# Performance work log

Hardware: AMD Instinct MI355X
Metric: run time of the kernel (lower is better)

The kernel has to match this reference:

```python
import jax, jax.numpy as jnp
import numpy as np

N_NODES = 100000


def _gcn_conv(x, w, b, edge_index, n):
    # Linear transform
    x = x @ w + b
    # Add self loops
    loops = jnp.tile(jnp.arange(n, dtype=edge_index.dtype), (2, 1))
    ei = jnp.concatenate([edge_index, loops], axis=1)
    src, tgt = ei[0], ei[1]
    # Degree of source nodes (every node has a self loop -> deg >= 1)
    deg = jax.ops.segment_sum(jnp.ones(src.shape, x.dtype), src, num_segments=n)
    dinv = deg ** -0.5
    norm = dinv[src] * dinv[tgt]  # [E+N]
    # Gather-scale-scatter: out[t] += norm_e * x[s]
    msgs = norm[:, None] * x[src]  # [E+N, out_ch]
    return jax.ops.segment_sum(msgs, tgt, num_segments=n)


def setup_inputs() -> dict:
    key = jax.random.key(0)
    ks = jax.random.split(key, 6)
    n, f_in, hid, n_cls, e = N_NODES, 512, 16, 40, 3200000
    x = jax.random.normal(ks[0], (n, f_in), dtype=jnp.float32)
    edge_index = jax.random.randint(ks[1], (2, e), 0, n, dtype=jnp.int64)
    w1 = jax.random.normal(ks[2], (f_in, hid), dtype=jnp.float32) * (1.0 / np.sqrt(f_in))
    b1 = jax.random.normal(ks[3], (hid,), dtype=jnp.float32) * 0.01
    w2 = jax.random.normal(ks[4], (hid, n_cls), dtype=jnp.float32) * (1.0 / np.sqrt(hid))
    b2 = jax.random.normal(ks[5], (n_cls,), dtype=jnp.float32) * 0.01
    return {"x": x, "edge_index": edge_index, "w1": w1, "b1": b1, "w2": w2, "b2": b2}


def reference(x, edge_index, w1, b1, w2, b2):
    n = x.shape[0]
    h = _gcn_conv(x, w1, b1, edge_index, n)
    h = jax.nn.relu(h)
    # dropout is identity in eval mode (F.dropout with training=False)
    h = _gcn_conv(h, w2, b2, edge_index, n)
    return jax.nn.log_softmax(h, axis=1)
```

## Files before the change

kernel.cpp:

```cpp
#include <hip/hip_runtime.h>
#include <hip/hip_fp16.h>
#include <cstdint>

#define FIN 512
#define HID 16
#define NCLS 40
#define SHIFT 8
#define NBCAP 512
#define NBLK 512
#define BR 64
#define KC 32
#define CAP 12288
#define FCAP 12288

typedef int   iv4 __attribute__((ext_vector_type(4)));
typedef float fv4 __attribute__((ext_vector_type(4)));



__global__ void zerocur_kernel(int* __restrict__ gcur) {
    int t = threadIdx.x;
    gcur[t] = 0;
    gcur[NBCAP + t] = 0;
}


__global__ void fused_scatter_kernel(const int* __restrict__ ei, int E, int nb,
                                     int* __restrict__ gcur,
                                     unsigned char* __restrict__ tmp_src,
                                     unsigned int* __restrict__ tmp_tgt) {
    __shared__ int hs[NBCAP], ht[NBCAP];
    int t = threadIdx.x;
    for (int j = t; j < NBCAP; j += 256) { hs[j] = 0; ht[j] = 0; }
    __syncthreads();
    if ((E & 3) == 0) {
        const iv4* s4 = (const iv4*)ei;
        const iv4* t4 = (const iv4*)(ei + E);
        int E4 = E >> 2;
        int per = (E4 + NBLK - 1) / NBLK;
        int lo = blockIdx.x * per;
        int hi = lo + per; if (hi > E4) hi = E4;
        for (int i = lo + t; i < hi; i += 256) {
            iv4 s = s4[i];
            iv4 tt = t4[i];
            atomicAdd(&hs[s.x >> SHIFT], 1); atomicAdd(&hs[s.y >> SHIFT], 1);
            atomicAdd(&hs[s.z >> SHIFT], 1); atomicAdd(&hs[s.w >> SHIFT], 1);
            atomicAdd(&ht[tt.x >> SHIFT], 1); atomicAdd(&ht[tt.y >> SHIFT], 1);
            atomicAdd(&ht[tt.z >> SHIFT], 1); atomicAdd(&ht[tt.w >> SHIFT], 1);
        }
        __syncthreads();
        for (int j = t; j < nb; j += 256) {
            int v = hs[j];
            int base = atomicAdd(&gcur[j], v);
            hs[j] = j * CAP + base;
            int w = ht[j];
            int baset = atomicAdd(&gcur[NBCAP + j], w);
            ht[j] = j * CAP + baset;
        }
        __syncthreads();
        for (int i = lo + t; i < hi; i += 256) {
            iv4 s = s4[i];
            iv4 tt = t4[i];
            int p;
            p = atomicAdd(&hs[s.x >> SHIFT], 1); tmp_src[p] = (unsigned char)(s.x & 255);
            p = atomicAdd(&hs[s.y >> SHIFT], 1); tmp_src[p] = (unsigned char)(s.y & 255);
            p = atomicAdd(&hs[s.z >> SHIFT], 1); tmp_src[p] = (unsigned char)(s.z & 255);
            p = atomicAdd(&hs[s.w >> SHIFT], 1); tmp_src[p] = (unsigned char)(s.w & 255);
            p = atomicAdd(&ht[tt.x >> SHIFT], 1); tmp_tgt[p] = ((unsigned int)(tt.x & 255) << 17) | (unsigned int)s.x;
            p = atomicAdd(&ht[tt.y >> SHIFT], 1); tmp_tgt[p] = ((unsigned int)(tt.y & 255) << 17) | (unsigned int)s.y;
            p = atomicAdd(&ht[tt.z >> SHIFT], 1); tmp_tgt[p] = ((unsigned int)(tt.z & 255) << 17) | (unsigned int)s.z;
            p = atomicAdd(&ht[tt.w >> SHIFT], 1); tmp_tgt[p] = ((unsigned int)(tt.w & 255) << 17) | (unsigned int)s.w;
        }
    } else {
        int per = (E + NBLK - 1) / NBLK;
        int lo = blockIdx.x * per;
        int hi = lo + per; if (hi > E) hi = E;
        for (int i = lo + t; i < hi; i += 256) {
            atomicAdd(&hs[ei[i] >> SHIFT], 1);
            atomicAdd(&ht[ei[E + i] >> SHIFT], 1);
        }
        __syncthreads();
        for (int j = t; j < nb; j += 256) {
            int v = hs[j];
            int base = atomicAdd(&gcur[j], v);
            hs[j] = j * CAP + base;
            int w = ht[j];
            int baset = atomicAdd(&gcur[NBCAP + j], w);
            ht[j] = j * CAP + baset;
        }
        __syncthreads();
        for (int i = lo + t; i < hi; i += 256) {
            int s = ei[i], tg = ei[E + i];
            int ps = atomicAdd(&hs[s >> SHIFT], 1);
            tmp_src[ps] = (unsigned char)(s & 255);
            int pt = atomicAdd(&ht[tg >> SHIFT], 1);
            tmp_tgt[pt] = ((unsigned int)(tg & 255) << 17) | (unsigned int)s;
        }
    }
}


__global__ void fine_kernel(const unsigned char* __restrict__ tmp_src,
                            const unsigned int* __restrict__ tmp_tgt,
                            const int* __restrict__ gcur,
                            float* __restrict__ dinv, int* __restrict__ row_ptr,
                            int* __restrict__ edges, int N, int E, int nb) {
    __shared__ unsigned int stage[FCAP];
    __shared__ int hist[256];
    __shared__ int h2[256];
    __shared__ int scan[256];
    int b = blockIdx.x;
    int t = threadIdx.x;
    int scnt = gcur[b];
    int cnt  = gcur[NBCAP + b];
    int sb0 = b * CAP;
    int part = 0;
    for (int j = t; j < b; j += 256) part += gcur[NBCAP + j];
    scan[t] = part;
    __syncthreads();
    for (int off = 128; off > 0; off >>= 1) {
        if (t < off) scan[t] += scan[t + off];
        __syncthreads();
    }
    int beg = scan[0];
    __syncthreads();
    bool staged = (cnt <= FCAP);
    hist[t] = 0;
    h2[t] = 0;
    __syncthreads();
    if (staged)
        for (int i = t; i < cnt; i += 256) stage[i] = __builtin_nontemporal_load(&tmp_tgt[sb0 + i]);
    for (int i = t; i < scnt; i += 256)
        atomicAdd(&hist[__builtin_nontemporal_load(&tmp_src[sb0 + i])], 1);
    __syncthreads();
    int node = b * 256 + t;
    if (node < N) dinv[node] = rsqrtf((float)(hist[t] + 1));
    if (staged) {
        for (int i = t; i < cnt; i += 256) atomicAdd(&h2[stage[i] >> 17], 1);
    } else {
        for (int i = t; i < cnt; i += 256) atomicAdd(&h2[__builtin_nontemporal_load(&tmp_tgt[sb0 + i]) >> 17], 1);
    }
    __syncthreads();
    int v = h2[t];
    scan[t] = v;
    __syncthreads();
    for (int off = 1; off < 256; off <<= 1) {
        int a = (t >= off) ? scan[t - off] : 0;
        __syncthreads();
        scan[t] += a;
        __syncthreads();
    }
    int ex = scan[t] - v;
    if (node < N) row_ptr[node] = beg + ex;
    if (b == nb - 1 && t == 0) row_ptr[N] = E;
    h2[t] = ex;
    __syncthreads();
    if (staged) {
        for (int i = t; i < cnt; i += 256) {
            unsigned int w = stage[i];
            int tl = (int)(w >> 17);
            edges[beg + atomicAdd(&h2[tl], 1)] = (int)(w & 0x1FFFF);
        }
    } else {
        for (int i = t; i < cnt; i += 256) {
            unsigned int w = __builtin_nontemporal_load(&tmp_tgt[sb0 + i]);
            int tl = (int)(w >> 17);
            edges[beg + atomicAdd(&h2[tl], 1)] = (int)(w & 0x1FFFF);
        }
    }
}


__global__ __launch_bounds__(256, 4)
void linear1_kernel(const float* __restrict__ x, const float* __restrict__ w1,
                    const float* __restrict__ b1, const float* __restrict__ dinv,
                    __half* __restrict__ h1h, int n) {
    __shared__ float xs[KC][BR + 2];
    __shared__ float wsc[KC * HID];
    __shared__ float bl[HID];
    int t = threadIdx.x;
    if (t < HID) bl[t] = b1[t];
    int row0 = blockIdx.x * BR;
    int rp = t >> 2;
    int cq = (t & 3) * 4;
    float acc[4] = {0, 0, 0, 0};

    fv4 xp[2];
    float wp[2];
    int rr_[2], kk_[2];
#pragma unroll
    for (int u = 0; u < 2; ++u) {
        int i = t + u * 256;
        rr_[u] = i >> 3;
        kk_[u] = (i & 7) * 4;
    }
    auto prefetch = [&](int kc) {
#pragma unroll
        for (int u = 0; u < 2; ++u) {
            int grow = row0 + rr_[u];
            if (grow < n) {
                xp[u] = __builtin_nontemporal_load((const fv4*)(x + (size_t)grow * FIN + kc + kk_[u]));
            } else {
                xp[u] = (fv4){0.f, 0.f, 0.f, 0.f};
            }
        }
        wp[0] = w1[kc * HID + t];
        wp[1] = w1[kc * HID + t + 256];
    };

    prefetch(0);
    for (int kc = 0; kc < FIN; kc += KC) {
        __syncthreads();
#pragma unroll
        for (int u = 0; u < 2; ++u) {
            xs[kk_[u] + 0][rr_[u]] = xp[u].x;
            xs[kk_[u] + 1][rr_[u]] = xp[u].y;
            xs[kk_[u] + 2][rr_[u]] = xp[u].z;
            xs[kk_[u] + 3][rr_[u]] = xp[u].w;
        }
        wsc[t] = wp[0];
        wsc[t + 256] = wp[1];
        __syncthreads();
        if (kc + KC < FIN) prefetch(kc + KC);
#pragma unroll 8
        for (int k = 0; k < KC; ++k) {
            float xv = xs[k][rp];
            float4 wv = *(const float4*)&wsc[k * HID + cq];
            acc[0] = fmaf(xv, wv.x, acc[0]);
            acc[1] = fmaf(xv, wv.y, acc[1]);
            acc[2] = fmaf(xv, wv.z, acc[2]);
            acc[3] = fmaf(xv, wv.w, acc[3]);
        }
    }
    int r0 = row0 + rp;
    if (r0 < n) {
        float dv = dinv[r0];
        __half2* hp = (__half2*)(h1h + (size_t)r0 * HID + cq);
        hp[0] = __floats2half2_rn(dv * (acc[0] + bl[cq + 0]), dv * (acc[1] + bl[cq + 1]));
        hp[1] = __floats2half2_rn(dv * (acc[2] + bl[cq + 2]), dv * (acc[3] + bl[cq + 3]));
    }
}


__global__ void agg1_kernel(const __half* __restrict__ in, const int* __restrict__ edges,
                            const int* __restrict__ row_ptr, const float* __restrict__ dinv,
                            __half* __restrict__ out16, float* __restrict__ rowsum, int n) {
    int gid = blockIdx.x * blockDim.x + threadIdx.x;
    int node = gid >> 5;
    int sub = (gid >> 3) & 3;
    int c2 = gid & 7;
    if (node >= n) return;
    const __half2* tab = (const __half2*)in;
    float dv = dinv[node];
    float a0 = 0.f, a1 = 0.f, rs = 0.f;
    if (sub == 0) {
        float2 sv = __half22float2(tab[(size_t)node * 8 + c2]);
        a0 = sv.x; a1 = sv.y; rs = dv;
    }
    int beg = row_ptr[node], end = row_ptr[node + 1];
#pragma unroll 4
    for (int i = beg + sub; i < end; i += 4) {
        int src = __builtin_nontemporal_load(&edges[i]);
        float2 v = __half22float2(tab[(size_t)src * 8 + c2]);
        a0 += v.x;
        a1 += v.y;
        rs += dinv[src];
    }
    a0 += __shfl_xor(a0, 8);  a1 += __shfl_xor(a1, 8);  rs += __shfl_xor(rs, 8);
    a0 += __shfl_xor(a0, 16); a1 += __shfl_xor(a1, 16); rs += __shfl_xor(rs, 16);
    if (sub == 0) {
        float dv2 = dv * dv;
        a0 = fmaxf(dv2 * a0, 0.f);
        a1 = fmaxf(dv2 * a1, 0.f);
        ((__half2*)out16)[(size_t)node * 8 + c2] = __floats2half2_rn(a0, a1);
        if (c2 == 0) rowsum[node] = dv * rs;
    }
}


__global__ void agg2_kernel(const __half* __restrict__ in, const int* __restrict__ edges,
                            const int* __restrict__ row_ptr, const float* __restrict__ dinv,
                            const float* __restrict__ rowsum,
                            const float* __restrict__ w2, const float* __restrict__ b2,
                            float* __restrict__ out, int n) {
    __shared__ float g2[8][HID + 1];
    __shared__ float wl[HID * NCLS];
    __shared__ float bl[NCLS];
    int t = threadIdx.x;
    for (int i = t; i < HID * NCLS; i += 256) wl[i] = w2[i];
    if (t < NCLS) bl[t] = b2[t];
    int gid = blockIdx.x * 256 + t;
    int node = gid >> 5;
    int sub = (t >> 3) & 3;
    int c2 = t & 7;
    int nl = t >> 5;
    float a0 = 0.f, a1 = 0.f;
    float dv = 0.f;
    if (node < n) {
        const __half2* tab = (const __half2*)in;
        dv = dinv[node];
        if (sub == 0) {
            float2 sv = __half22float2(tab[(size_t)node * 8 + c2]);
            a0 = sv.x; a1 = sv.y;
        }
        int beg = row_ptr[node], end = row_ptr[node + 1];
#pragma unroll 4
        for (int i = beg + sub; i < end; i += 4) {
            int src = __builtin_nontemporal_load(&edges[i]);
            float2 v = __half22float2(tab[(size_t)src * 8 + c2]);
            a0 += v.x;
            a1 += v.y;
        }
    }
    a0 += __shfl_xor(a0, 8);  a1 += __shfl_xor(a1, 8);
    a0 += __shfl_xor(a0, 16); a1 += __shfl_xor(a1, 16);
    if (sub == 0) { g2[nl][c2 * 2] = dv * a0; g2[nl][c2 * 2 + 1] = dv * a1; }
    __syncthreads();
    if (t < 16) {
        int nl2 = t >> 1, half = t & 1;
        int node2 = blockIdx.x * 8 + nl2;
        float z[20];
        float m = -1e30f, se = 0.f;
        if (node2 < n) {
            float h[HID];
#pragma unroll
            for (int j = 0; j < HID; ++j) h[j] = g2[nl2][j];
            float rs = rowsum[node2];
            int c0 = half * 20;
#pragma unroll
            for (int c = 0; c < 20; ++c) {
                float s = rs * bl[c0 + c];
#pragma unroll
                for (int j = 0; j < HID; ++j) s = fmaf(h[j], wl[j * NCLS + c0 + c], s);
                z[c] = s;
            }
            m = z[0];
#pragma unroll
            for (int c = 1; c < 20; ++c) m = fmaxf(m, z[c]);
        }
        m = fmaxf(m, __shfl_xor(m, 1));
        if (node2 < n) {
#pragma unroll
            for (int c = 0; c < 20; ++c) se += __expf(z[c] - m);
        }
        se += __shfl_xor(se, 1);
        if (node2 < n) {
            float lse = m + __logf(se);
            float* orow = out + (size_t)node2 * NCLS + half * 20;
#pragma unroll
            for (int c = 0; c < 20; ++c) orow[c] = z[c] - lse;
        }
    }
}


extern "C" void kernel_launch(void* const* d_in, const int* in_sizes, int n_in,
                              void* d_out, int out_size, void* d_ws, size_t ws_size,
                              hipStream_t stream) {
    const float* x  = (const float*)d_in[0];
    const int*   ei = (const int*)d_in[1];
    const float* w1 = (const float*)d_in[2];
    const float* b1 = (const float*)d_in[3];
    const float* w2 = (const float*)d_in[4];
    const float* b2 = (const float*)d_in[5];
    float* out = (float*)d_out;

    int N = in_sizes[0] / FIN;
    int E = in_sizes[1] / 2;
    int nb = (N + 255) >> SHIFT;

    char* p = (char*)d_ws;
    auto alloc = [&](size_t bytes) -> char* {
        char* r = p;
        p += (bytes + 255) / 256 * 256;
        return r;
    };
    int*   gcur      = (int*)alloc((size_t)2 * NBCAP * 4);
    float* dinv      = (float*)alloc((size_t)N * 4);
    int*   row_ptr   = (int*)alloc((size_t)(N + 1) * 4);
    unsigned char* tmp_src = (unsigned char*)alloc((size_t)nb * CAP);
    unsigned int*  tmp_tgt = (unsigned int*)alloc((size_t)nb * CAP * 4);
    int*    edges    = (int*)alloc((size_t)E * 4);
    __half* h1h      = (__half*)alloc((size_t)N * HID * 2);
    __half* gh       = (__half*)alloc((size_t)N * HID * 2);
    float*  rowsum   = (float*)alloc((size_t)N * 4);

    zerocur_kernel<<<1, NBCAP, 0, stream>>>(gcur);
    fused_scatter_kernel<<<NBLK, 256, 0, stream>>>(ei, E, nb, gcur, tmp_src, tmp_tgt);
    fine_kernel<<<nb, 256, 0, stream>>>(tmp_src, tmp_tgt, gcur,
                                        dinv, row_ptr, edges, N, E, nb);
    linear1_kernel<<<(N + BR - 1) / BR, 256, 0, stream>>>(x, w1, b1, dinv, h1h, N);
    agg1_kernel<<<(N * 32 + 255) / 256, 256, 0, stream>>>(h1h, edges, row_ptr, dinv,
                                                          gh, rowsum, N);
    agg2_kernel<<<(N * 32 + 255) / 256, 256, 0, stream>>>(gh, edges, row_ptr, dinv,
                                                          rowsum, w2, b2, out, N);
}
```

Measured before the change: 511.9 us.

## Drop CSR build; aggregate from coarse buckets with shared-memory atomics

Removes the fine CSR construction (row_ptr/edges scatter and scans) and keeps only a degree histogram kernel, which now reads source bytes four at a time. Both aggregation kernels now use one 1024-thread block per 256-node target bucket and read the bucketed tmp_tgt entries directly. Each block accumulates neighbor features into shared memory with float atomics, then applies normalization, ReLU and the output epilogue. This saves a kernel and an edge-array write/read pass, at the cost of heavy LDS atomic contention, nondeterministic summation order and only about 391 blocks per launch.

```diff
diff --git a/kernel.cpp b/kernel.cpp
--- a/kernel.cpp
+++ b/kernel.cpp
@@ -11,7 +11,6 @@
 #define BR 64
 #define KC 32
 #define CAP 12288
-#define FCAP 12288
 
 typedef int   iv4 __attribute__((ext_vector_type(4)));
 typedef float fv4 __attribute__((ext_vector_type(4)));
@@ -100,74 +99,28 @@
 }
 
 
-__global__ void fine_kernel(const unsigned char* __restrict__ tmp_src,
-                            const unsigned int* __restrict__ tmp_tgt,
+__global__ void dinv_kernel(const unsigned char* __restrict__ tmp_src,
                             const int* __restrict__ gcur,
-                            float* __restrict__ dinv, int* __restrict__ row_ptr,
-                            int* __restrict__ edges, int N, int E, int nb) {
-    __shared__ unsigned int stage[FCAP];
+                            float* __restrict__ dinv, int N) {
     __shared__ int hist[256];
-    __shared__ int h2[256];
-    __shared__ int scan[256];
-    int b = blockIdx.x;
-    int t = threadIdx.x;
+    int b = blockIdx.x, t = threadIdx.x;
+    hist[t] = 0;
+    __syncthreads();
     int scnt = gcur[b];
-    int cnt  = gcur[NBCAP + b];
-    int sb0 = b * CAP;
-    int part = 0;
-    for (int j = t; j < b; j += 256) part += gcur[NBCAP + j];
-    scan[t] = part;
-    __syncthreads();
-    for (int off = 128; off > 0; off >>= 1) {
-        if (t < off) scan[t] += scan[t + off];
-        __syncthreads();
-    }
-    int beg = scan[0];
-    __syncthreads();
-    bool staged = (cnt <= FCAP);
-    hist[t] = 0;
-    h2[t] = 0;
-    __syncthreads();
-    if (staged)
-        for (int i = t; i < cnt; i += 256) stage[i] = __builtin_nontemporal_load(&tmp_tgt[sb0 + i]);
-    for (int i = t; i < scnt; i += 256)
-        atomicAdd(&hist[__builtin_nontemporal_load(&tmp_src[sb0 + i])], 1);
+    const unsigned int* sp = (const unsigned int*)(tmp_src + (size_t)b * CAP);
+    int s4n = scnt >> 2;
+    for (int i = t; i < s4n; i += 256) {
+        unsigned int w = sp[i];
+        atomicAdd(&hist[w & 255], 1);
+        atomicAdd(&hist[(w >> 8) & 255], 1);
+        atomicAdd(&hist[(w >> 16) & 255], 1);
+        atomicAdd(&hist[w >> 24], 1);
+    }
+    for (int i = (s4n << 2) + t; i < scnt; i += 256)
+        atomicAdd(&hist[tmp_src[(size_t)b * CAP + i]], 1);
     __syncthreads();
     int node = b * 256 + t;
     if (node < N) dinv[node] = rsqrtf((float)(hist[t] + 1));
-    if (staged) {
-        for (int i = t; i < cnt; i += 256) atomicAdd(&h2[stage[i] >> 17], 1);
-    } else {
-        for (int i = t; i < cnt; i += 256) atomicAdd(&h2[__builtin_nontemporal_load(&tmp_tgt[sb0 + i]) >> 17], 1);
-    }
-    __syncthreads();
-    int v = h2[t];
-    scan[t] = v;
-    __syncthreads();
-    for (int off = 1; off < 256; off <<= 1) {
-        int a = (t >= off) ? scan[t - off] : 0;
-        __syncthreads();
-        scan[t] += a;
-        __syncthreads();
-    }
-    int ex = scan[t] - v;
-    if (node < N) row_ptr[node] = beg + ex;
-    if (b == nb - 1 && t == 0) row_ptr[N] = E;
-    h2[t] = ex;
-    __syncthreads();
-    if (staged) {
-        for (int i = t; i < cnt; i += 256) {
-            unsigned int w = stage[i];
-            int tl = (int)(w >> 17);
-            edges[beg + atomicAdd(&h2[tl], 1)] = (int)(w & 0x1FFFF);
-        }
-    } else {
-        for (int i = t; i < cnt; i += 256) {
-            unsigned int w = __builtin_nontemporal_load(&tmp_tgt[sb0 + i]);
-            int tl = (int)(w >> 17);
-            edges[beg + atomicAdd(&h2[tl], 1)] = (int)(w & 0x1FFFF);
-        }
-    }
 }
 
 
@@ -242,91 +195,96 @@
 }
 
 
-__global__ void agg1_kernel(const __half* __restrict__ in, const int* __restrict__ edges,
-                            const int* __restrict__ row_ptr, const float* __restrict__ dinv,
-                            __half* __restrict__ out16, float* __restrict__ rowsum, int n) {
-    int gid = blockIdx.x * blockDim.x + threadIdx.x;
-    int node = gid >> 5;
-    int sub = (gid >> 3) & 3;
-    int c2 = gid & 7;
-    if (node >= n) return;
+__global__ __launch_bounds__(1024, 4)
+void agg1_kernel(const __half* __restrict__ in,
+                 const unsigned int* __restrict__ tmp_tgt,
+                 const int* __restrict__ gcur,
+                 const float* __restrict__ dinv,
+                 __half* __restrict__ gh, float* __restrict__ rowsum, int n) {
+    __shared__ float acc[256 * 17];
+    int b = blockIdx.x;
+    int t = threadIdx.x;
+    for (int j = t; j < 256 * 17; j += 1024) acc[j] = 0.f;
+    __syncthreads();
+    int cnt = gcur[NBCAP + b];
+    size_t base = (size_t)b * CAP;
+    int slot = t >> 3;
+    int c2 = t & 7;
     const __half2* tab = (const __half2*)in;
-    float dv = dinv[node];
-    float a0 = 0.f, a1 = 0.f, rs = 0.f;
-    if (sub == 0) {
-        float2 sv = __half22float2(tab[(size_t)node * 8 + c2]);
-        a0 = sv.x; a1 = sv.y; rs = dv;
-    }
-    int beg = row_ptr[node], end = row_ptr[node + 1];
-#pragma unroll 4
-    for (int i = beg + sub; i < end; i += 4) {
-        int src = __builtin_nontemporal_load(&edges[i]);
+    for (int i = slot; i < cnt; i += 128) {
+        unsigned int w = tmp_tgt[base + i];
+        int tl = (int)(w >> 17);
+        int src = (int)(w & 0x1FFFF);
         float2 v = __half22float2(tab[(size_t)src * 8 + c2]);
-        a0 += v.x;
-        a1 += v.y;
-        rs += dinv[src];
-    }
-    a0 += __shfl_xor(a0, 8);  a1 += __shfl_xor(a1, 8);  rs += __shfl_xor(rs, 8);
-    a0 += __shfl_xor(a0, 16); a1 += __shfl_xor(a1, 16); rs += __shfl_xor(rs, 16);
-    if (sub == 0) {
+        atomicAdd(&acc[tl * 17 + 2 * c2], v.x);
+        atomicAdd(&acc[tl * 17 + 2 * c2 + 1], v.y);
+        if (c2 == 0) atomicAdd(&acc[tl * 17 + 16], dinv[src]);
+    }
+    __syncthreads();
+    int node = b * 256 + t;
+    if (t < 256 && node < n) {
+        float dv = dinv[node];
         float dv2 = dv * dv;
-        a0 = fmaxf(dv2 * a0, 0.f);
-        a1 = fmaxf(dv2 * a1, 0.f);
-        ((__half2*)out16)[(size_t)node * 8 + c2] = __floats2half2_rn(a0, a1);
-        if (c2 == 0) rowsum[node] = dv * rs;
-    }
-}
-
-
-__global__ void agg2_kernel(const __half* __restrict__ in, const int* __restrict__ edges,
-                            const int* __restrict__ row_ptr, const float* __restrict__ dinv,
-                            const float* __restrict__ rowsum,
-                            const float* __restrict__ w2, const float* __restrict__ b2,
-                            float* __restrict__ out, int n) {
-    __shared__ float g2[8][HID + 1];
+        const __half2* hp = tab + (size_t)node * 8;
+        __half2* gp = (__half2*)gh + (size_t)node * 8;
+#pragma unroll
+        for (int c = 0; c < 8; ++c) {
+            float2 sv = __half22float2(hp[c]);
+            float a0 = fmaxf(dv2 * (sv.x + acc[t * 17 + 2 * c]), 0.f);
+            float a1 = fmaxf(dv2 * (sv.y + acc[t * 17 + 2 * c + 1]), 0.f);
+            gp[c] = __floats2half2_rn(a0, a1);
+        }
+        rowsum[node] = dv * (dv + acc[t * 17 + 16]);
+    }
+}
+
+
+__global__ __launch_bounds__(1024, 4)
+void agg2_kernel(const __half* __restrict__ in,
+                 const unsigned int* __restrict__ tmp_tgt,
+                 const int* __restrict__ gcur,
+                 const float* __restrict__ dinv,
+                 const float* __restrict__ rowsum,
+                 const float* __restrict__ w2, const float* __restrict__ b2,
+                 float* __restrict__ out, int n) {
+    __shared__ float acc[256 * 17];
     __shared__ float wl[HID * NCLS];
     __shared__ float bl[NCLS];
     int t = threadIdx.x;
-    for (int i = t; i < HID * NCLS; i += 256) wl[i] = w2[i];
+    for (int i = t; i < HID * NCLS; i += 1024) wl[i] = w2[i];
     if (t < NCLS) bl[t] = b2[t];
-    int gid = blockIdx.x * 256 + t;
-    int node = gid >> 5;
-    int sub = (t >> 3) & 3;
-    int c2 = t & 7;
-    int nl = t >> 5;
-    float a0 = 0.f, a1 = 0.f;
-    float dv = 0.f;
-    if (node < n) {
-        const __half2* tab = (const __half2*)in;
-        dv = dinv[node];
-        if (sub == 0) {
-            float2 sv = __half22float2(tab[(size_t)node * 8 + c2]);
-            a0 = sv.x; a1 = sv.y;
-        }
-        int beg = row_ptr[node], end = row_ptr[node + 1];
-#pragma unroll 4
-        for (int i = beg + sub; i < end; i += 4) {
-            int src = __builtin_nontemporal_load(&edges[i]);
-            float2 v = __half22float2(tab[(size_t)src * 8 + c2]);
-            a0 += v.x;
-            a1 += v.y;
-        }
-    }
-    a0 += __shfl_xor(a0, 8);  a1 += __shfl_xor(a1, 8);
-    a0 += __shfl_xor(a0, 16); a1 += __shfl_xor(a1, 16);
-    if (sub == 0) { g2[nl][c2 * 2] = dv * a0; g2[nl][c2 * 2 + 1] = dv * a1; }
-    __syncthreads();
-    if (t < 16) {
+    for (int j = t; j < 256 * 17; j += 1024) acc[j] = 0.f;
+    __syncthreads();
+    int b = blockIdx.x;
+    int cnt = gcur[NBCAP + b];
+    size_t base = (size_t)b * CAP;
+    int slot = t >> 3, c2 = t & 7;
+    const __half2* tab = (const __half2*)in;
+    for (int i = slot; i < cnt; i += 128) {
+        unsigned int w = tmp_tgt[base + i];
+        int tl = (int)(w >> 17);
+        int src = (int)(w & 0x1FFFF);
+        float2 v = __half22float2(tab[(size_t)src * 8 + c2]);
+        atomicAdd(&acc[tl * 17 + 2 * c2], v.x);
+        atomicAdd(&acc[tl * 17 + 2 * c2 + 1], v.y);
+    }
+    __syncthreads();
+    if (t < 512) {
         int nl2 = t >> 1, half = t & 1;
-        int node2 = blockIdx.x * 8 + nl2;
-        float z[20];
-        float m = -1e30f, se = 0.f;
-        if (node2 < n) {
+        int node = b * 256 + nl2;
+        if (node < n) {
+            float dv = dinv[node];
+            const __half2* hp = tab + (size_t)node * 8;
             float h[HID];
 #pragma unroll
-            for (int j = 0; j < HID; ++j) h[j] = g2[nl2][j];
-            float rs = rowsum[node2];
+            for (int c = 0; c < 8; ++c) {
+                float2 sv = __half22float2(hp[c]);
+                h[2 * c]     = dv * (sv.x + acc[nl2 * 17 + 2 * c]);
+                h[2 * c + 1] = dv * (sv.y + acc[nl2 * 17 + 2 * c + 1]);
+            }
+            float rs = rowsum[node];
             int c0 = half * 20;
+            float z[20];
 #pragma unroll
             for (int c = 0; c < 20; ++c) {
                 float s = rs * bl[c0 + c];
@@ -334,19 +292,16 @@
                 for (int j = 0; j < HID; ++j) s = fmaf(h[j], wl[j * NCLS + c0 + c], s);
                 z[c] = s;
             }
-            m = z[0];
+            float m = z[0];
 #pragma unroll
             for (int c = 1; c < 20; ++c) m = fmaxf(m, z[c]);
-        }
-        m = fmaxf(m, __shfl_xor(m, 1));
-        if (node2 < n) {
+            m = fmaxf(m, __shfl_xor(m, 1));
+            float se = 0.f;
 #pragma unroll
             for (int c = 0; c < 20; ++c) se += __expf(z[c] - m);
-        }
-        se += __shfl_xor(se, 1);
-        if (node2 < n) {
+            se += __shfl_xor(se, 1);
             float lse = m + __logf(se);
-            float* orow = out + (size_t)node2 * NCLS + half * 20;
+            float* orow = out + (size_t)node * NCLS + c0;
 #pragma unroll
             for (int c = 0; c < 20; ++c) orow[c] = z[c] - lse;
         }
@@ -377,21 +332,16 @@
     };
     int*   gcur      = (int*)alloc((size_t)2 * NBCAP * 4);
     float* dinv      = (float*)alloc((size_t)N * 4);
-    int*   row_ptr   = (int*)alloc((size_t)(N + 1) * 4);
     unsigned char* tmp_src = (unsigned char*)alloc((size_t)nb * CAP);
     unsigned int*  tmp_tgt = (unsigned int*)alloc((size_t)nb * CAP * 4);
-    int*    edges    = (int*)alloc((size_t)E * 4);
     __half* h1h      = (__half*)alloc((size_t)N * HID * 2);
     __half* gh       = (__half*)alloc((size_t)N * HID * 2);
     float*  rowsum   = (float*)alloc((size_t)N * 4);
 
     zerocur_kernel<<<1, NBCAP, 0, stream>>>(gcur);
     fused_scatter_kernel<<<NBLK, 256, 0, stream>>>(ei, E, nb, gcur, tmp_src, tmp_tgt);
-    fine_kernel<<<nb, 256, 0, stream>>>(tmp_src, tmp_tgt, gcur,
-                                        dinv, row_ptr, edges, N, E, nb);
+    dinv_kernel<<<nb, 256, 0, stream>>>(tmp_src, gcur, dinv, N);
     linear1_kernel<<<(N + BR - 1) / BR, 256, 0, stream>>>(x, w1, b1, dinv, h1h, N);
-    agg1_kernel<<<(N * 32 + 255) / 256, 256, 0, stream>>>(h1h, edges, row_ptr, dinv,
-                                                          gh, rowsum, N);
-    agg2_kernel<<<(N * 32 + 255) / 256, 256, 0, stream>>>(gh, edges, row_ptr, dinv,
-                                                          rowsum, w2, b2, out, N);
-}
+    agg1_kernel<<<nb, 1024, 0, stream>>>(h1h, tmp_tgt, gcur, dinv, gh, rowsum, N);
+    agg2_kernel<<<nb, 1024, 0, stream>>>(gh, tmp_tgt, gcur, dinv, rowsum, w2, b2, out, N);
+}
```

New measurement: 1.068 ms. 109% more time.
